# Performance work log

Measured on AMD Instinct MI355X. Metric: run time of the kernel, lower is better.

The kernel has to match this reference:

```python
import jax, jax.numpy as jnp
import numpy as np
from jax import lax

B, IMG, C = 128, 224, 3
P0, P1 = 16, 8
N0 = (IMG // P0) ** 2   # 196
N1 = (IMG // P1) ** 2   # 784
D0 = C * P0 * P0        # 768
BN_EPS = 1e-3           # Keras BatchNormalization default epsilon


def patchify(x, p):
    """[B,H,W,C] -> [B,(H/p)*(W/p),p,p,C], row-major patch order (matches tf split/stack)."""
    b, h, w, c = x.shape
    x = x.reshape(b, h // p, p, w // p, p, c).transpose(0, 1, 3, 2, 4, 5)
    return x.reshape(b, (h // p) * (w // p), p, p, c)


def unpatchify(x):
    """[B,N,h,w,C] -> [B,h*e,w*e,C] with e=sqrt(N); inverse of patchify."""
    b, n, h, w, c = x.shape
    e = int(np.sqrt(n))
    x = x.reshape(b, e, e, h, w, c).transpose(0, 1, 3, 2, 4, 5)
    return x.reshape(b, e * h, e * w, c)


def setup_inputs() -> dict:
    key = jax.random.key(0)
    k0, k1, k2 = jax.random.split(key, 3)
    return {
        "X": jax.random.normal(k0, (B, IMG, IMG, C), jnp.float32),
        "pos_emb": jax.random.normal(k1, (N0, D0), jnp.float32) * 0.02,
        "conv_w": jax.random.normal(k2, (2, 2, N0, N1), jnp.float32) * 0.02,  # HWIO
        "bn_gamma": jnp.ones((N1,), jnp.float32),
        "bn_beta": jnp.zeros((N1,), jnp.float32),
        "bn_mean": jnp.zeros((N1,), jnp.float32),
        "bn_var": jnp.ones((N1,), jnp.float32),
    }


def reference(X, pos_emb, conv_w, bn_gamma, bn_beta, bn_mean, bn_var):
    # 1) patchify at coarse scale and add position embedding
    enc = patchify(X, P0).reshape(B, N0, D0) + pos_emb          # [B,N0,768]
    enc = enc.reshape(B, N0, P0, P0, C)                          # [B,196,16,16,3]

    # 2) position pipeline: treat patches-as-channels image [C,P0,P0,N0],
    #    Conv2D(N1, k=2, s=2, SAME, no bias) + inference BatchNorm
    pos_img = pos_emb.reshape(N0, P0, P0, C).transpose(3, 1, 2, 0)  # [3,16,16,196]
    pos_c = lax.conv_general_dilated(
        pos_img, conv_w, window_strides=(2, 2), padding="SAME",
        dimension_numbers=("NHWC", "HWIO", "NHWC"))                 # [3,8,8,784]
    pos_c = (pos_c - bn_mean) * (bn_gamma / jnp.sqrt(bn_var + BN_EPS)) + bn_beta
    pos_new = pos_c.transpose(3, 1, 2, 0)                           # [N1,P1,P1,C]

    # 3) resample encoded patches 16 -> 8 (unpatch to image, re-patch), add positions
    enc = patchify(unpatchify(enc), P1)                          # [B,784,8,8,3]
    enc = enc + pos_new[None]

    # 4) final resample 8 -> 16 and flatten
    out = patchify(unpatchify(enc), P0).reshape(B, N0, D0)       # [B,196,768]
    return out
```

## Files before the change

### kernel.cpp

```cpp
#include <hip/hip_runtime.h>


#define TOT_BIAS (3 * 8 * 8 * 784)
#define TOT_OUT (128 * 196 * 768)
#define TOT_OUT4 (TOT_OUT / 4)

__global__ void __launch_bounds__(256) compute_bias_kernel(
    const float* __restrict__ pos_emb,
    const float* __restrict__ conv_w,
    const float* __restrict__ bn_gamma,
    const float* __restrict__ bn_beta,
    const float* __restrict__ bn_mean,
    const float* __restrict__ bn_var,
    float* __restrict__ bias)
{
    int idx = blockIdx.x * blockDim.x + threadIdx.x;
    if (idx >= TOT_BIAS) return;
    int o = idx % 784;
    int t = idx / 784;
    int j = t % 8;
    t /= 8;
    int i = t % 8;
    int c = t / 8;

    float sum = 0.f;
#pragma unroll
    for (int di = 0; di < 2; ++di) {
#pragma unroll
        for (int dj = 0; dj < 2; ++dj) {
            const int y16 = 2 * i + di;
            const int x16 = 2 * j + dj;
            const int pe_off = (y16 * 16 + x16) * 3 + c;
            const float* __restrict__ w = conv_w + (size_t)((di * 2 + dj) * 196) * 784 + o;
            for (int n = 0; n < 196; ++n) {
                sum += pos_emb[n * 768 + pe_off] * w[(size_t)n * 784];
            }
        }
    }

    const float scale = bn_gamma[o] / sqrtf(bn_var[o] + 1e-3f);
    const float val = (sum - bn_mean[o]) * scale + bn_beta[o];

    const int y8 = o / 28, x8 = o % 28;
    const int y = y8 * 8 + i;
    const int x = x8 * 8 + j;
    const int n0 = (y >> 4) * 14 + (x >> 4);
    const int py = y & 15, px = x & 15;
    const int d = (py * 16 + px) * 3 + c;
    bias[n0 * 768 + d] = pos_emb[n0 * 768 + d] + val;
}

__global__ void __launch_bounds__(256) add_bias_kernel(
    const float* __restrict__ X,
    const float* __restrict__ bias,
    float* __restrict__ out)
{
    int tid = blockIdx.x * blockDim.x + threadIdx.x;
    if (tid >= TOT_OUT4) return;
    const int flat = tid * 4;
    const int b = flat / 150528;
    const int rem = flat - b * 150528;
    const int n0 = rem / 768;
    const int d = rem - n0 * 768;
    const int py = d / 48;
    const int r = d - py * 48;
    const int y = (n0 / 14) * 16 + py;
    const int xcol = (n0 % 14) * 48 + r;
    const float4 xv = *reinterpret_cast<const float4*>(X + (size_t)b * 150528 + y * 672 + xcol);
    const float4 bv = *reinterpret_cast<const float4*>(bias + rem);
    float4 ov;
    ov.x = xv.x + bv.x;
    ov.y = xv.y + bv.y;
    ov.z = xv.z + bv.z;
    ov.w = xv.w + bv.w;
    *reinterpret_cast<float4*>(out + flat) = ov;
}

extern "C" void kernel_launch(void* const* d_in, const int* in_sizes, int n_in,
                              void* d_out, int out_size, void* d_ws, size_t ws_size,
                              hipStream_t stream) {
    const float* X        = (const float*)d_in[0];
    const float* pos_emb  = (const float*)d_in[1];
    const float* conv_w   = (const float*)d_in[2];
    const float* bn_gamma = (const float*)d_in[3];
    const float* bn_beta  = (const float*)d_in[4];
    const float* bn_mean  = (const float*)d_in[5];
    const float* bn_var   = (const float*)d_in[6];
    float* out  = (float*)d_out;
    float* bias = (float*)d_ws;

    compute_bias_kernel<<<(TOT_BIAS + 255) / 256, 256, 0, stream>>>(
        pos_emb, conv_w, bn_gamma, bn_beta, bn_mean, bn_var, bias);
    add_bias_kernel<<<(TOT_OUT4 + 255) / 256, 256, 0, stream>>>(X, bias, out);
}
```

Measured before the change: 209.6 us.

## Tile conv-bias computation with shared-memory staging and split-K over taps

Rewrites the positional conv+BN bias kernel so each block stages the needed pos_emb values in shared memory and each thread computes four output columns. The 784-long reduction is split across the four conv taps by separate thread groups and then combined through shared memory. This is meant to cut redundant strided global loads, reuse each conv weight load four times, and shorten the serial FMA dependency chain. It adds two block barriers and an extra shared-memory reduction step.

```diff
diff --git a/kernel.cpp b/kernel.cpp
--- a/kernel.cpp
+++ b/kernel.cpp
@@ -1,11 +1,10 @@
 #include <hip/hip_runtime.h>
 
 
-#define TOT_BIAS (3 * 8 * 8 * 784)
 #define TOT_OUT (128 * 196 * 768)
 #define TOT_OUT4 (TOT_OUT / 4)
 
-__global__ void __launch_bounds__(256) compute_bias_kernel(
+__global__ void __launch_bounds__(256) compute_bias_v2(
     const float* __restrict__ pos_emb,
     const float* __restrict__ conv_w,
     const float* __restrict__ bn_gamma,
@@ -14,40 +13,72 @@
     const float* __restrict__ bn_var,
     float* __restrict__ bias)
 {
-    int idx = blockIdx.x * blockDim.x + threadIdx.x;
-    if (idx >= TOT_BIAS) return;
-    int o = idx % 784;
-    int t = idx / 784;
-    int j = t % 8;
-    t /= 8;
-    int i = t % 8;
-    int c = t / 8;
+    __shared__ float At[784 * 4];
+    __shared__ float4 red[4][64];
 
-    float sum = 0.f;
+    const int mg = blockIdx.x;
+    const int ot = blockIdx.y;
+    const int c  = mg >> 4;
+    const int i  = (mg & 15) >> 1;
+    const int j0 = (mg & 1) * 4;
+    const int t  = threadIdx.x;
+
+    for (int idx = t; idx < 784 * 4; idx += 256) {
+        const int ml  = idx & 3;
+        const int k   = idx >> 2;
+        const int tap = k / 196;
+        const int n   = k - tap * 196;
+        const int di = tap >> 1, dj = tap & 1;
+        const int y16 = 2 * i + di;
+        const int x16 = 2 * (j0 + ml) + dj;
+        At[idx] = pos_emb[n * 768 + (y16 * 16 + x16) * 3 + c];
+    }
+    __syncthreads();
+
+    const int o_lane = t & 63;
+    const int tap    = t >> 6;
+    const int o      = ot * 64 + o_lane;
+    const int o_c    = o < 784 ? o : 783;
+    const float* __restrict__ wp = conv_w + (size_t)(tap * 196) * 784 + o_c;
+    const float4* __restrict__ At4 = reinterpret_cast<const float4*>(At) + tap * 196;
+
+    float4 acc = {0.f, 0.f, 0.f, 0.f};
+#pragma unroll 4
+    for (int n = 0; n < 196; ++n) {
+        const float  wv = wp[n * 784];
+        const float4 a  = At4[n];
+        acc.x += a.x * wv;
+        acc.y += a.y * wv;
+        acc.z += a.z * wv;
+        acc.w += a.w * wv;
+    }
+    red[tap][o_lane] = acc;
+    __syncthreads();
+
+    if (t < 64) {
+        const int oo = ot * 64 + t;
+        if (oo < 784) {
+            const float4 r0 = red[0][t], r1 = red[1][t], r2 = red[2][t], r3 = red[3][t];
+            float sum[4];
+            sum[0] = r0.x + r1.x + r2.x + r3.x;
+            sum[1] = r0.y + r1.y + r2.y + r3.y;
+            sum[2] = r0.z + r1.z + r2.z + r3.z;
+            sum[3] = r0.w + r1.w + r2.w + r3.w;
+            const float scale = bn_gamma[oo] * rsqrtf(bn_var[oo] + 1e-3f);
+            const float mb = bn_mean[oo], bb = bn_beta[oo];
+            const int y8 = oo / 28, x8 = oo % 28;
 #pragma unroll
-    for (int di = 0; di < 2; ++di) {
-#pragma unroll
-        for (int dj = 0; dj < 2; ++dj) {
-            const int y16 = 2 * i + di;
-            const int x16 = 2 * j + dj;
-            const int pe_off = (y16 * 16 + x16) * 3 + c;
-            const float* __restrict__ w = conv_w + (size_t)((di * 2 + dj) * 196) * 784 + o;
-            for (int n = 0; n < 196; ++n) {
-                sum += pos_emb[n * 768 + pe_off] * w[(size_t)n * 784];
+            for (int ml = 0; ml < 4; ++ml) {
+                const float val = (sum[ml] - mb) * scale + bb;
+                const int j = j0 + ml;
+                const int y = y8 * 8 + i;
+                const int x = x8 * 8 + j;
+                const int n0 = (y >> 4) * 14 + (x >> 4);
+                const int d  = ((y & 15) * 16 + (x & 15)) * 3 + c;
+                bias[n0 * 768 + d] = pos_emb[n0 * 768 + d] + val;
             }
         }
     }
-
-    const float scale = bn_gamma[o] / sqrtf(bn_var[o] + 1e-3f);
-    const float val = (sum - bn_mean[o]) * scale + bn_beta[o];
-
-    const int y8 = o / 28, x8 = o % 28;
-    const int y = y8 * 8 + i;
-    const int x = x8 * 8 + j;
-    const int n0 = (y >> 4) * 14 + (x >> 4);
-    const int py = y & 15, px = x & 15;
-    const int d = (py * 16 + px) * 3 + c;
-    bias[n0 * 768 + d] = pos_emb[n0 * 768 + d] + val;
 }
 
 __global__ void __launch_bounds__(256) add_bias_kernel(
@@ -89,7 +120,8 @@
     float* out  = (float*)d_out;
     float* bias = (float*)d_ws;
 
-    compute_bias_kernel<<<(TOT_BIAS + 255) / 256, 256, 0, stream>>>(
+    dim3 bias_grid(48, 13);
+    compute_bias_v2<<<bias_grid, 256, 0, stream>>>(
         pos_emb, conv_w, bn_gamma, bn_beta, bn_mean, bn_var, bias);
     add_bias_kernel<<<(TOT_OUT4 + 255) / 256, 256, 0, stream>>>(X, bias, out);
 }
```

Result: faster. 173.9 us (-17.0%).
